# Kernel tuning notes

Measured on AMD Instinct MI355X. Metric: run time of the kernel, lower is better.

## Reference

```python
import jax, jax.numpy as jnp
import numpy as np

B = 1024      # number of samples (sample_idx.shape[0])
H = 256       # hidden_size
E = 64        # number of observation events
NO = 512      # observed samples per event
D = 16        # input_size
ND = 2        # n_dim
S = 4         # euler ODE steps between consecutive events
EPS = 1e-8


def setup_inputs() -> dict:
    key = jax.random.key(0)
    ks = jax.random.split(key, 24)
    X = jax.random.normal(ks[0], (E, NO, D, ND), jnp.float32)
    M = jnp.ones((E, NO, D), jnp.float32)
    rng = np.random.default_rng(0)
    # distinct indices per event (torch scatter temp[i_obs]=... assumes no dup within event)
    batch_idx = jnp.asarray(
        np.stack([rng.permutation(B)[:NO] for _ in range(E)]).astype(np.int32))
    dt = jnp.float32(0.05)
    s = 1.0 / np.sqrt(H)
    def U(k, shp):
        return jax.random.uniform(k, shp, jnp.float32, -s, s)
    inp = {"X": X, "M": M, "batch_idx": batch_idx, "dt": dt}
    # GRU-ODE cell (3 Linear layers H->H, bias init 0.01 in torch; random here)
    inp["ode_Wr"], inp["ode_br"] = U(ks[1], (H, H)), U(ks[2], (H,))
    inp["ode_Wz"], inp["ode_bz"] = U(ks[3], (H, H)), U(ks[4], (H,))
    inp["ode_Wh"], inp["ode_bh"] = U(ks[5], (H, H)), U(ks[6], (H,))
    # GRUCell for observation update: input size 2*D, hidden H
    inp["g_Wxr"], inp["g_Wxz"], inp["g_Wxn"] = U(ks[7], (2 * D, H)), U(ks[8], (2 * D, H)), U(ks[9], (2 * D, H))
    inp["g_Uhr"], inp["g_Uhz"], inp["g_Uhn"] = U(ks[10], (H, H)), U(ks[11], (H, H)), U(ks[12], (H, H))
    inp["g_bxr"], inp["g_bxz"], inp["g_bxn"] = U(ks[13], (H,)), U(ks[14], (H,)), U(ks[15], (H,))
    inp["g_bhr"], inp["g_bhz"], inp["g_bhn"] = U(ks[16], (H,)), U(ks[17], (H,)), U(ks[18], (H,))
    # p_model: Linear(H,H) -> ReLU -> (Dropout p=0, identity in eval) -> Linear(H, D-1)
    inp["p_W1"], inp["p_b1"] = U(ks[19], (H, H)), U(ks[20], (H,))
    inp["p_W2"], inp["p_b2"] = U(ks[21], (H, D - 1)), U(ks[22], (D - 1,))
    return inp


def reference(X, M, batch_idx, dt,
              ode_Wr, ode_br, ode_Wz, ode_bz, ode_Wh, ode_bh,
              g_Wxr, g_Wxz, g_Wxn, g_Uhr, g_Uhz, g_Uhn,
              g_bxr, g_bxz, g_bxn, g_bhr, g_bhz, g_bhn,
              p_W1, p_b1, p_W2, p_b2):
    def euler_step(h):
        r = jax.nn.sigmoid(h @ ode_Wr + ode_br)
        z = jax.nn.sigmoid(h @ ode_Wz + ode_bz)
        u = jnp.tanh((r * h) @ ode_Wh + ode_bh)
        return h + dt * (1.0 - z) * (u - h)

    def event_step(carry, xs):
        h, mse, mae, mape, tot = carry
        Xe, Me, ie = xs                      # [NO,D,ND], [NO,D], [NO]
        for _ in range(S):                   # ODE evolution up to this obs time
            h = euler_step(h)
        p = jax.nn.relu(h @ p_W1 + p_b1) @ p_W2 + p_b2   # [B, D-1]
        Xt = Xe[:, 1:, 0]                    # X_obs[:, :, 0][:, 1:]
        Mt = Me[:, 1:]
        diff = Xt - p[ie]
        mse = mse + jnp.sum(diff * diff * Mt)
        mae = mae + jnp.sum(jnp.abs(diff) * Mt)
        mape = mape + jnp.sum(jnp.abs(diff) / (Xt + EPS) * Mt)
        tot = tot + jnp.sum(Mt)
        # GRUCell observation update, scattered back into h
        x_in = Xe.reshape(Xe.shape[0], -1)   # [NO, 2*D]
        hi = h[ie]                           # [NO, H]
        r = jax.nn.sigmoid(x_in @ g_Wxr + g_bxr + hi @ g_Uhr + g_bhr)
        z = jax.nn.sigmoid(x_in @ g_Wxz + g_bxz + hi @ g_Uhz + g_bhz)
        n = jnp.tanh(x_in @ g_Wxn + g_bxn + r * (hi @ g_Uhn + g_bhn))
        hn = (1.0 - z) * n + z * hi
        h = h.at[ie].set(hn)
        return (h, mse, mae, mape, tot), None

    h0 = jnp.zeros((B, H), jnp.float32)
    zero = jnp.float32(0.0)
    (h, mse, mae, mape, tot), _ = jax.lax.scan(
        event_step, (h0, zero, zero, zero, zero), (X, M, batch_idx))
    return (mse / tot, mae / tot, mape / tot)
```

## Files before the change

kernel.cpp:

```cpp
#include <hip/hip_runtime.h>

#define Bv 1024
#define Ev 64
#define NOv 512
#define L2E  1.44269504088896340736f
#define L2E2 2.88539008177792681472f

typedef _Float16 h8 __attribute__((ext_vector_type(8)));
typedef float f32x4 __attribute__((ext_vector_type(4)));
typedef int i32x8 __attribute__((ext_vector_type(8)));

#define LDH8 272
#define LDA1 264
#define LDX  48

#define MF16(a,b,c) __builtin_amdgcn_mfma_f32_16x16x32_f16((a),(b),(c),0,0,0)
#define MFS(a,b,c) __builtin_amdgcn_mfma_scale_f32_16x16x128_f8f6f4((a),(b),(c),0,0,0,0x7F7F7F7F,0,0x7F7F7F7F)

__device__ __forceinline__ float rcpf(float x) {
    float r; asm("v_rcp_f32 %0, %1" : "=v"(r) : "v"(x)); return r;
}
__device__ __forceinline__ float ex2(float x) {
    float r; asm("v_exp_f32 %0, %1" : "=v"(r) : "v"(x)); return r;
}
__device__ __forceinline__ float sig2(float y) { return rcpf(1.0f + ex2(-y)); }
__device__ __forceinline__ float tanh2(float y) { return fmaf(2.0f, sig2(y), -1.0f); }
__device__ __forceinline__ int pk4_fp8(float a, float b, float c, float d) {
    int p = __builtin_amdgcn_cvt_pk_fp8_f32(a, b, 0, false);
    p = __builtin_amdgcn_cvt_pk_fp8_f32(c, d, p, true);
    return p;
}
__device__ __forceinline__ char fp8b(float v) {
    return (char)(__builtin_amdgcn_cvt_pk_fp8_f32(v, v, 0, false) & 0xff);
}
#define GATHER(dst, A) { \
    float lo_ = sA ? A[1] : A[0]; \
    float hi_ = sA ? A[3] : A[2]; \
    dst = sB ? hi_ : lo_; }

__device__ __forceinline__ i32x8 ld8(const int4* __restrict__ A,
                                     const int4* __restrict__ B, int idx) {
    int4 lo = A[idx], hi = B[idx];
    i32x8 w;
    w[0] = lo.x; w[1] = lo.y; w[2] = lo.z; w[3] = lo.w;
    w[4] = hi.x; w[5] = hi.y; w[6] = hi.z; w[7] = hi.w;
    return w;
}

__device__ __forceinline__ void pack8_body(const float* __restrict__ src,
                                           int4* __restrict__ dst,
                                           int idx, float scale) {
    int lane = idx & 63;
    int kh = (idx >> 6) & 1;
    int ct = idx >> 7;
    int k0 = kh * 128 + (lane >> 4) * 32;
    int n = ct * 16 + (lane & 15);
    int w[8];
    #pragma unroll
    for (int q = 0; q < 8; ++q) {
        float s[4];
        #pragma unroll
        for (int j = 0; j < 4; ++j)
            s[j] = scale * src[(k0 + q * 4 + j) * 256 + n];
        w[q] = pk4_fp8(s[0], s[1], s[2], s[3]);
    }
    dst[idx * 2]     = make_int4(w[0], w[1], w[2], w[3]);
    dst[idx * 2 + 1] = make_int4(w[4], w[5], w[6], w[7]);
}
__device__ __forceinline__ void pack16_body(const float* __restrict__ src,
                                            _Float16* __restrict__ dst,
                                            int idx, int KS, int ncols, float scale) {
    int lane = idx & 63;
    int ks = (idx >> 6) % KS;
    int ct = (idx >> 6) / KS;
    int k0 = ks * 32 + (lane >> 4) * 8;
    int n = ct * 16 + (lane & 15);
    h8 v;
    #pragma unroll
    for (int j = 0; j < 8; ++j)
        v[j] = (n < ncols) ? (_Float16)(scale * src[(k0 + j) * ncols + n]) : (_Float16)0.f;
    ((h8*)dst)[idx] = v;
}

__global__ void prep_all(
    const float* __restrict__ Wr,  const float* __restrict__ Wz,  const float* __restrict__ Wh,
    const float* __restrict__ Uhr, const float* __restrict__ Uhz, const float* __restrict__ Uhn,
    const float* __restrict__ W1,
    const float* __restrict__ Wxr, const float* __restrict__ Wxz, const float* __restrict__ Wxn,
    const float* __restrict__ W2,
    int4* __restrict__ WrQ,  int4* __restrict__ WzQ,  int4* __restrict__ WhQ,
    int4* __restrict__ UhrQ, int4* __restrict__ UhzQ, int4* __restrict__ UhnQ,
    int4* __restrict__ W1Q,
    _Float16* __restrict__ WxrH, _Float16* __restrict__ WxzH, _Float16* __restrict__ WxnH,
    _Float16* __restrict__ W2H,
    int* __restrict__ inv)
{
    int b = blockIdx.x, tid = threadIdx.x;
    if (b < 56) {
        int g = b >> 3;
        int idx = (b & 7) * 256 + tid;
        const float* src; int4* dst; float sc;
        switch (g) {
            case 0: src = Wr;  dst = WrQ;  sc = L2E;  break;
            case 1: src = Wz;  dst = WzQ;  sc = L2E;  break;
            case 2: src = Wh;  dst = WhQ;  sc = L2E2; break;
            case 3: src = Uhr; dst = UhrQ; sc = L2E;  break;
            case 4: src = Uhz; dst = UhzQ; sc = L2E;  break;
            case 5: src = Uhn; dst = UhnQ; sc = L2E2; break;
            default: src = W1; dst = W1Q;  sc = 1.0f; break;
        }
        pack8_body(src, dst, idx, sc);
    } else if (b < 68) {
        int g = (b - 56) >> 2;
        int idx = ((b - 56) & 3) * 256 + tid;
        const float* src; _Float16* dst; float sc;
        switch (g) {
            case 0: src = Wxr; dst = WxrH; sc = L2E;  break;
            case 1: src = Wxz; dst = WxzH; sc = L2E;  break;
            default: src = Wxn; dst = WxnH; sc = L2E2; break;
        }
        pack16_body(src, dst, idx, 1, 256, sc);
    } else if (b < 70) {
        int idx = (b - 68) * 256 + tid;
        if (idx < 512) pack16_body(W2, W2H, idx, 8, 15, 1.0f);
    } else {
        int i = (b - 70) * 256 + tid;
        if (i < Ev * Bv) inv[i] = -1;
    }
}

__global__ void gather_all(const float* __restrict__ X, const float* __restrict__ M,
                           const int* __restrict__ bidx,
                           int* __restrict__ inv, _Float16* __restrict__ Xg,
                           float* __restrict__ Tx, float* __restrict__ Tm)
{
    int b = blockIdx.x, tid = threadIdx.x;
    if (b < 128) {
        int i = b * 256 + tid;
        if (i < Ev * NOv) {
            int e = i >> 9;
            int o = i & (NOv - 1);
            inv[e * Bv + bidx[i]] = o;
        }
    } else if (b < 4224) {
        int i = (b - 128) * 256 + tid;
        if (i < Ev * NOv * 32) {
            int q = i & 31, o = (i >> 5) & (NOv - 1), e = i >> 14;
            int bb = bidx[e * NOv + o];
            Xg[(e * Bv + bb) * 32 + q] = (_Float16)X[i];
        }
    } else {
        int i = (b - 4224) * 256 + tid;
        if (i < Ev * NOv * 16) {
            int m = i & 15, o = (i >> 4) & (NOv - 1), e = i >> 13;
            int bb = bidx[e * NOv + o];
            int d = (e * Bv + bb) * 16 + m;
            if (m < 15) {
                Tx[d] = X[((e * NOv + o) * 16 + 1 + m) * 2];
                Tm[d] = M[(e * NOv + o) * 16 + 1 + m];
            } else {
                Tx[d] = 1.f;
                Tm[d] = 0.f;
            }
        }
    }
}

__global__ __launch_bounds__(1024) void gruode_main(
    const _Float16* __restrict__ Xg, const float* __restrict__ Tx, const float* __restrict__ Tm,
    const float* __restrict__ dtp,
    const float* __restrict__ br, const float* __restrict__ bz, const float* __restrict__ bh,
    const float* __restrict__ bxr, const float* __restrict__ bxz, const float* __restrict__ bxn,
    const float* __restrict__ bhr, const float* __restrict__ bhz, const float* __restrict__ bhn,
    const float* __restrict__ b1, const float* __restrict__ b2,
    const i32x8* __restrict__ WrQ, const i32x8* __restrict__ WzQ, const i32x8* __restrict__ WhQ,
    const i32x8* __restrict__ UhrQ, const i32x8* __restrict__ UhzQ, const i32x8* __restrict__ UhnQ,
    const i32x8* __restrict__ W1Q,
    const h8* __restrict__ WxrH, const h8* __restrict__ WxzH, const h8* __restrict__ WxnH,
    const h8* __restrict__ W2H,
    const int* __restrict__ inv, double* __restrict__ partials)
{
    __shared__ __align__(16) int4     UhrA[2048], UhrB[2048];
    __shared__ __align__(16) int4     UhzA[2048], UhzB[2048];
    __shared__ __align__(16) h8       W2L[512];
    __shared__ __align__(16) char     hb2[2][4 * LDH8];
    __shared__ __align__(16) _Float16 a1s[4 * LDA1];
    __shared__ __align__(16) _Float16 x16d[2][4 * LDX];
    __shared__ __align__(16) float    bias_s[5][256];
    __shared__ __align__(16) float    b2s[16];
    __shared__ int    obsi2[2][16];
    __shared__ double wred[16][4];

    const int tid  = threadIdx.x;
    const int lane = tid & 63;
    const int wid  = tid >> 6;
    const int l16  = lane & 15;
    const int lg   = lane >> 4;
    const int n0   = wid * 16 + lg * 4;
    const int row0 = blockIdx.x * 4;
    const float dtv = dtp[0];
    const int rrow = l16 & 3;

    const int rho = lane & 3;
    const int kap = lane >> 2;
    const int gam = wid * 16 + kap;
    const int hoff = rho * LDH8 + gam;
    const bool sA = (kap & 1) != 0;
    const bool sB = (kap & 2) != 0;
    const int sbase = 64 * lg + 4 * rrow;

    if (tid < 256) {
        bias_s[0][tid] = (bxr[tid] + bhr[tid]) * L2E;
        bias_s[1][tid] = (bxz[tid] + bhz[tid]) * L2E;
        bias_s[2][tid] = bxn[tid] * L2E2;
    } else if (tid < 512) {
        int t = tid - 256;
        bias_s[3][t] = bhn[t] * L2E2;
        bias_s[4][t] = b1[t];
    }
    if (tid < 16) b2s[tid] = (tid < 15) ? b2[tid] : 0.f;
    if (tid < LDH8) {
        ((int*)hb2[0])[tid] = 0;
        ((int*)hb2[1])[tid] = 0;
    }
    for (int i = tid; i < 2048; i += 1024) {
        const int4* s1 = (const int4*)&UhrQ[i];
        UhrA[i] = s1[0]; UhrB[i] = s1[1];
        const int4* s2 = (const int4*)&UhzQ[i];
        UhzA[i] = s2[0]; UhzB[i] = s2[1];
    }
    if (tid < 512) W2L[tid] = W2H[tid];
    if (tid < 16) obsi2[0][tid] = (tid < 4) ? inv[row0 + tid] : -1;
    if (tid < 128) {
        int row = tid >> 5, q = tid & 31;
        x16d[0][row * LDX + q] = Xg[(row0 + row) * 32 + q];
    }

    const float bRs = br[gam] * L2E;
    const float bZs = bz[gam] * L2E;
    const float bUs = bh[gam] * L2E2;

    i32x8 wr0 = WrQ[(wid * 2 + 0) * 64 + lane], wr1 = WrQ[(wid * 2 + 1) * 64 + lane];
    i32x8 wz0 = WzQ[(wid * 2 + 0) * 64 + lane], wz1 = WzQ[(wid * 2 + 1) * 64 + lane];
    i32x8 wh0 = WhQ[(wid * 2 + 0) * 64 + lane], wh1 = WhQ[(wid * 2 + 1) * 64 + lane];

    float hs = 0.f;
    double am0 = 0.0, am1 = 0.0, am2 = 0.0, am3 = 0.0;
    const f32x4 zf = {0.f, 0.f, 0.f, 0.f};
    __syncthreads();

    #pragma unroll 1
    for (int e = 0; e < Ev; ++e) {
        char* __restrict__ HB = hb2[e & 1];
        char* __restrict__ RB = hb2[(e & 1) ^ 1];
        const _Float16* __restrict__ xs = x16d[e & 1];
        const int* __restrict__ obs = obsi2[e & 1];

        float zs = 0.f;
        for (int s = 0; s < 4; ++s) {
            f32x4 aR = zf, aZ = zf;
            {
                i32x8 hb = *(const i32x8*)&HB[rrow * LDH8 + lg * 32];
                aR = MFS(wr0, hb, aR); aZ = MFS(wz0, hb, aZ);
                hb = *(const i32x8*)&HB[rrow * LDH8 + 128 + lg * 32];
                aR = MFS(wr1, hb, aR); aZ = MFS(wz1, hb, aZ);
            }
            float rpre, zpre;
            GATHER(rpre, aR);
            GATHER(zpre, aZ);
            float rv = sig2(rpre + bRs);
            zs = sig2(zpre + bZs);
            RB[hoff] = fp8b(rv * hs);
            __syncthreads();
            f32x4 aU0 = zf, aU1 = zf;
            {
                i32x8 rb = *(const i32x8*)&RB[rrow * LDH8 + lg * 32];
                aU0 = MFS(wh0, rb, aU0);
                rb = *(const i32x8*)&RB[rrow * LDH8 + 128 + lg * 32];
                aU1 = MFS(wh1, rb, aU1);
            }
            float u0, u1;
            GATHER(u0, aU0);
            GATHER(u1, aU1);
            float u = tanh2(u0 + u1 + bUs);
            hs = hs + dtv * (1.f - zs) * (u - hs);
            HB[hoff] = fp8b(hs);
            __syncthreads();
        }
        __builtin_amdgcn_sched_barrier(0);

        i32x8 hb0 = *(const i32x8*)&HB[rrow * LDH8 + lg * 32];
        i32x8 hb1 = *(const i32x8*)&HB[rrow * LDH8 + 128 + lg * 32];
        f32x4 aN = *(const f32x4*)&bias_s[3][n0];
        {
            f32x4 aW = *(const f32x4*)&bias_s[4][n0];
            aN = MFS(UhnQ[(wid * 2 + 0) * 64 + lane], hb0, aN);
            aW = MFS(W1Q[(wid * 2 + 0) * 64 + lane], hb0, aW);
            aN = MFS(UhnQ[(wid * 2 + 1) * 64 + lane], hb1, aN);
            aW = MFS(W1Q[(wid * 2 + 1) * 64 + lane], hb1, aW);
            if (l16 < 4) {
                _Float16 a1v[4];
                #pragma unroll
                for (int r = 0; r < 4; ++r)
                    a1v[r] = (_Float16)fmaxf(aW[r], 0.f);
                *(long*)&a1s[l16 * LDA1 + n0] = *(const long*)a1v;
            }
        }
        {
            int en = (e + 1 < Ev) ? e + 1 : e;
            int nb = (e + 1) & 1;
            if (tid < 16) obsi2[nb][tid] = (tid < 4) ? inv[en * Bv + row0 + tid] : -1;
            if (tid < 128) {
                int row = tid >> 5, q = tid & 31;
                x16d[nb][row * LDX + q] = Xg[(en * Bv + row0 + row) * 32 + q];
            }
        }
        float4 txv = {0.f,0.f,0.f,0.f}, tmv = {0.f,0.f,0.f,0.f};
        if (wid == 0) {
            int gr = row0 + l16; if (gr > Bv - 1) gr = Bv - 1;
            txv = *(const float4*)&Tx[(e * Bv + gr) * 16 + lg * 4];
            tmv = *(const float4*)&Tm[(e * Bv + gr) * 16 + lg * 4];
        }
        float rg[4];
        {
            f32x4 aG = *(const f32x4*)&bias_s[0][n0];
            aG = MFS(ld8(UhrA, UhrB, (wid * 2 + 0) * 64 + lane), hb0, aG);
            aG = MFS(ld8(UhrA, UhrB, (wid * 2 + 1) * 64 + lane), hb1, aG);
            h8 bx = *(const h8*)&xs[rrow * LDX + lg * 8];
            aG = MF16(WxrH[wid * 64 + lane], bx, aG);
            #pragma unroll
            for (int r = 0; r < 4; ++r)
                rg[r] = sig2(aG[r]);
        }
        {
            f32x4 aG = *(const f32x4*)&bias_s[1][n0];
            aG = MFS(ld8(UhzA, UhzB, (wid * 2 + 0) * 64 + lane), hb0, aG);
            aG = MFS(ld8(UhzA, UhzB, (wid * 2 + 1) * 64 + lane), hb1, aG);
            h8 bx = *(const h8*)&xs[rrow * LDX + lg * 8];
            aG = MF16(WxzH[wid * 64 + lane], bx, aG);
            f32x4 aNx = *(const f32x4*)&bias_s[2][n0];
            aNx = MF16(WxnH[wid * 64 + lane], bx, aNx);
            float how[4];
            #pragma unroll
            for (int r = 0; r < 4; ++r)
                how[r] = __int_as_float(__builtin_amdgcn_ds_bpermute(sbase + 16 * r, __float_as_int(hs)));
            float hn[4];
            #pragma unroll
            for (int r = 0; r < 4; ++r) {
                float zg = sig2(aG[r]);
                float nv = tanh2(aNx[r] + rg[r] * aN[r]);
                hn[r] = (1.f - zg) * nv + zg * how[r];
            }
            float hng;
            GATHER(hng, hn);
            if (obs[rho] >= 0) hs = hng;
            RB[hoff] = fp8b(hs);
        }
        __syncthreads();
        if (wid == 0) {
            f32x4 aP = *(const f32x4*)&b2s[lg * 4];
            f32x4 aQ = zf;
            #pragma unroll
            for (int ks = 0; ks < 4; ++ks) {
                h8 ba = *(const h8*)&a1s[rrow * LDA1 + (2 * ks) * 32 + lg * 8];
                aP = MF16(W2L[(2 * ks) * 64 + lane], ba, aP);
                h8 bb = *(const h8*)&a1s[rrow * LDA1 + (2 * ks + 1) * 32 + lg * 8];
                aQ = MF16(W2L[(2 * ks + 1) * 64 + lane], bb, aQ);
            }
            if (obs[l16] >= 0) {
                float m0 = 0.f, m1 = 0.f, m2 = 0.f, m3 = 0.f;
                #pragma unroll
                for (int r = 0; r < 4; ++r) {
                    float p  = aP[r] + aQ[r];
                    float xt = ((const float*)&txv)[r];
                    float mt = ((const float*)&tmv)[r];
                    float diff = xt - p;
                    m0 += diff * diff * mt;
                    m1 += fabsf(diff) * mt;
                    m2 += fabsf(diff) * rcpf(xt + 1e-8f) * mt;
                    m3 += mt;
                }
                am0 += (double)m0;
                am1 += (double)m1;
                am2 += (double)m2;
                am3 += (double)m3;
            }
        }
    }

    __syncthreads();
    double v[4] = {am0, am1, am2, am3};
    #pragma unroll
    for (int m = 0; m < 4; ++m) {
        double t = v[m];
        for (int off = 32; off; off >>= 1) t += __shfl_down(t, off);
        if (lane == 0) wred[wid][m] = t;
    }
    __syncthreads();
    if (tid == 0) {
        for (int m = 0; m < 4; ++m) {
            double t = 0.0;
            for (int w = 0; w < 16; ++w) t += wred[w][m];
            partials[blockIdx.x * 4 + m] = t;
        }
    }
}

__global__ void finalize_k(const double* __restrict__ partials, float* __restrict__ out) {
    __shared__ double sd[4][4];
    int t = threadIdx.x;
    int l = t & 63, w = t >> 6;
    double v0 = partials[t * 4 + 0];
    double v1 = partials[t * 4 + 1];
    double v2 = partials[t * 4 + 2];
    double v3 = partials[t * 4 + 3];
    for (int off = 32; off; off >>= 1) {
        v0 += __shfl_down(v0, off);
        v1 += __shfl_down(v1, off);
        v2 += __shfl_down(v2, off);
        v3 += __shfl_down(v3, off);
    }
    if (l == 0) { sd[w][0] = v0; sd[w][1] = v1; sd[w][2] = v2; sd[w][3] = v3; }
    __syncthreads();
    if (t == 0) {
        double r0 = 0, r1 = 0, r2 = 0, r3 = 0;
        for (int i = 0; i < 4; ++i) { r0 += sd[i][0]; r1 += sd[i][1]; r2 += sd[i][2]; r3 += sd[i][3]; }
        out[0] = (float)(r0 / r3);
        out[1] = (float)(r1 / r3);
        out[2] = (float)(r2 / r3);
    }
}

extern "C" void kernel_launch(void* const* d_in, const int* in_sizes, int n_in,
                              void* d_out, int out_size, void* d_ws, size_t ws_size,
                              hipStream_t stream) {
    const float* X   = (const float*)d_in[0];
    const float* M   = (const float*)d_in[1];
    const int*  bidx = (const int*)d_in[2];
    const float* dtp = (const float*)d_in[3];
    const float* Wr  = (const float*)d_in[4];
    const float* brr = (const float*)d_in[5];
    const float* Wz  = (const float*)d_in[6];
    const float* bzz = (const float*)d_in[7];
    const float* Wh  = (const float*)d_in[8];
    const float* bhh = (const float*)d_in[9];
    const float* Wxr = (const float*)d_in[10];
    const float* Wxz = (const float*)d_in[11];
    const float* Wxn = (const float*)d_in[12];
    const float* Uhr = (const float*)d_in[13];
    const float* Uhz = (const float*)d_in[14];
    const float* Uhn = (const float*)d_in[15];
    const float* bxr = (const float*)d_in[16];
    const float* bxz = (const float*)d_in[17];
    const float* bxn = (const float*)d_in[18];
    const float* bhr = (const float*)d_in[19];
    const float* bhz = (const float*)d_in[20];
    const float* bhn = (const float*)d_in[21];
    const float* W1  = (const float*)d_in[22];
    const float* b1  = (const float*)d_in[23];
    const float* W2  = (const float*)d_in[24];
    const float* b2  = (const float*)d_in[25];

    char* w = (char*)d_ws;
    i32x8* WrQ  = (i32x8*)(w + 0 * 65536);
    i32x8* WzQ  = (i32x8*)(w + 1 * 65536);
    i32x8* WhQ  = (i32x8*)(w + 2 * 65536);
    i32x8* UhrQ = (i32x8*)(w + 3 * 65536);
    i32x8* UhzQ = (i32x8*)(w + 4 * 65536);
    i32x8* UhnQ = (i32x8*)(w + 5 * 65536);
    i32x8* W1Q  = (i32x8*)(w + 6 * 65536);
    _Float16* WxrH = (_Float16*)(w + 458752);
    _Float16* WxzH = (_Float16*)(w + 475136);
    _Float16* WxnH = (_Float16*)(w + 491520);
    _Float16* W2H  = (_Float16*)(w + 507904);
    int* inv = (int*)(w + 516096);
    _Float16* Xg = (_Float16*)(w + 778240);
    float* Tx = (float*)(w + 4972544);
    float* Tm = (float*)(w + 9166848);
    double* partials = (double*)(w + 13361152);

    prep_all<<<326, 256, 0, stream>>>(
        Wr, Wz, Wh, Uhr, Uhz, Uhn, W1, Wxr, Wxz, Wxn, W2,
        (int4*)WrQ, (int4*)WzQ, (int4*)WhQ, (int4*)UhrQ, (int4*)UhzQ,
        (int4*)UhnQ, (int4*)W1Q, WxrH, WxzH, WxnH, W2H, inv);
    gather_all<<<6272, 256, 0, stream>>>(X, M, bidx, inv, Xg, Tx, Tm);

    gruode_main<<<256, 1024, 0, stream>>>(Xg, Tx, Tm, dtp,
        brr, bzz, bhh, bxr, bxz, bxn, bhr, bhz, bhn, b1, b2,
        WrQ, WzQ, WhQ, UhrQ, UhzQ, UhnQ, W1Q,
        (const h8*)WxrH, (const h8*)WxzH, (const h8*)WxnH, (const h8*)W2H,
        inv, partials);

    finalize_k<<<1, 256, 0, stream>>>(partials, (float*)d_out);
}
```

Measured before the change: 441.7 us.

## Halve rows per block, double grid, and stream Uhr/Uhz weights from global

Each block now handles 2 sample rows instead of 4, and the grid doubles to 512 blocks so the 64-event recurrence is spread over more workgroups. The 128 KB LDS staging of the Uhr/Uhz fp8 weights is removed; those MFMA operands are read directly from global memory, with scheduling barriers placed around the gate blocks. The finalize kernel sums 512 partial results instead of 256. The intent is more parallelism per CU at lower LDS use. The costs are that only 2 of the 16 MFMA rows now carry data, the weight reads go through global memory and cache rather than LDS, and if two 1024-thread blocks cannot share a CU, the extra blocks run as a second serial wave.

```diff
diff --git a/kernel.cpp b/kernel.cpp
--- a/kernel.cpp
+++ b/kernel.cpp
@@ -37,15 +37,6 @@
     float lo_ = sA ? A[1] : A[0]; \
     float hi_ = sA ? A[3] : A[2]; \
     dst = sB ? hi_ : lo_; }
-
-__device__ __forceinline__ i32x8 ld8(const int4* __restrict__ A,
-                                     const int4* __restrict__ B, int idx) {
-    int4 lo = A[idx], hi = B[idx];
-    i32x8 w;
-    w[0] = lo.x; w[1] = lo.y; w[2] = lo.z; w[3] = lo.w;
-    w[4] = hi.x; w[5] = hi.y; w[6] = hi.z; w[7] = hi.w;
-    return w;
-}
 
 __device__ __forceinline__ void pack8_body(const float* __restrict__ src,
                                            int4* __restrict__ dst,
@@ -180,12 +171,10 @@
     const h8* __restrict__ W2H,
     const int* __restrict__ inv, double* __restrict__ partials)
 {
-    __shared__ __align__(16) int4     UhrA[2048], UhrB[2048];
-    __shared__ __align__(16) int4     UhzA[2048], UhzB[2048];
     __shared__ __align__(16) h8       W2L[512];
-    __shared__ __align__(16) char     hb2[2][4 * LDH8];
-    __shared__ __align__(16) _Float16 a1s[4 * LDA1];
-    __shared__ __align__(16) _Float16 x16d[2][4 * LDX];
+    __shared__ __align__(16) char     hb2[2][2 * LDH8];
+    __shared__ __align__(16) _Float16 a1s[2 * LDA1];
+    __shared__ __align__(16) _Float16 x16d[2][2 * LDX];
     __shared__ __align__(16) float    bias_s[5][256];
     __shared__ __align__(16) float    b2s[16];
     __shared__ int    obsi2[2][16];
@@ -197,14 +186,14 @@
     const int l16  = lane & 15;
     const int lg   = lane >> 4;
     const int n0   = wid * 16 + lg * 4;
-    const int row0 = blockIdx.x * 4;
+    const int row0 = blockIdx.x * 2;
     const float dtv = dtp[0];
-    const int rrow = l16 & 3;
-
-    const int rho = lane & 3;
+    const int rrow = l16 & 1;
+
+    const int rho2 = lane & 1;
     const int kap = lane >> 2;
     const int gam = wid * 16 + kap;
-    const int hoff = rho * LDH8 + gam;
+    const int hoff = rho2 * LDH8 + gam;
     const bool sA = (kap & 1) != 0;
     const bool sB = (kap & 2) != 0;
     const int sbase = 64 * lg + 4 * rrow;
@@ -219,19 +208,13 @@
         bias_s[4][t] = b1[t];
     }
     if (tid < 16) b2s[tid] = (tid < 15) ? b2[tid] : 0.f;
-    if (tid < LDH8) {
+    if (tid < 136) {
         ((int*)hb2[0])[tid] = 0;
         ((int*)hb2[1])[tid] = 0;
     }
-    for (int i = tid; i < 2048; i += 1024) {
-        const int4* s1 = (const int4*)&UhrQ[i];
-        UhrA[i] = s1[0]; UhrB[i] = s1[1];
-        const int4* s2 = (const int4*)&UhzQ[i];
-        UhzA[i] = s2[0]; UhzB[i] = s2[1];
-    }
     if (tid < 512) W2L[tid] = W2H[tid];
-    if (tid < 16) obsi2[0][tid] = (tid < 4) ? inv[row0 + tid] : -1;
-    if (tid < 128) {
+    if (tid < 16) obsi2[0][tid] = (tid < 2) ? inv[row0 + tid] : -1;
+    if (tid < 64) {
         int row = tid >> 5, q = tid & 31;
         x16d[0][row * LDX + q] = Xg[(row0 + row) * 32 + q];
     }
@@ -298,7 +281,7 @@
             aW = MFS(W1Q[(wid * 2 + 0) * 64 + lane], hb0, aW);
             aN = MFS(UhnQ[(wid * 2 + 1) * 64 + lane], hb1, aN);
             aW = MFS(W1Q[(wid * 2 + 1) * 64 + lane], hb1, aW);
-            if (l16 < 4) {
+            if (l16 < 2) {
                 _Float16 a1v[4];
                 #pragma unroll
                 for (int r = 0; r < 4; ++r)
@@ -309,8 +292,8 @@
         {
             int en = (e + 1 < Ev) ? e + 1 : e;
             int nb = (e + 1) & 1;
-            if (tid < 16) obsi2[nb][tid] = (tid < 4) ? inv[en * Bv + row0 + tid] : -1;
-            if (tid < 128) {
+            if (tid < 16) obsi2[nb][tid] = (tid < 2) ? inv[en * Bv + row0 + tid] : -1;
+            if (tid < 64) {
                 int row = tid >> 5, q = tid & 31;
                 x16d[nb][row * LDX + q] = Xg[(en * Bv + row0 + row) * 32 + q];
             }
@@ -321,21 +304,23 @@
             txv = *(const float4*)&Tx[(e * Bv + gr) * 16 + lg * 4];
             tmv = *(const float4*)&Tm[(e * Bv + gr) * 16 + lg * 4];
         }
+        __builtin_amdgcn_sched_barrier(0);
         float rg[4];
         {
             f32x4 aG = *(const f32x4*)&bias_s[0][n0];
-            aG = MFS(ld8(UhrA, UhrB, (wid * 2 + 0) * 64 + lane), hb0, aG);
-            aG = MFS(ld8(UhrA, UhrB, (wid * 2 + 1) * 64 + lane), hb1, aG);
+            aG = MFS(UhrQ[(wid * 2 + 0) * 64 + lane], hb0, aG);
+            aG = MFS(UhrQ[(wid * 2 + 1) * 64 + lane], hb1, aG);
             h8 bx = *(const h8*)&xs[rrow * LDX + lg * 8];
             aG = MF16(WxrH[wid * 64 + lane], bx, aG);
             #pragma unroll
             for (int r = 0; r < 4; ++r)
                 rg[r] = sig2(aG[r]);
         }
+        __builtin_amdgcn_sched_barrier(0);
         {
             f32x4 aG = *(const f32x4*)&bias_s[1][n0];
-            aG = MFS(ld8(UhzA, UhzB, (wid * 2 + 0) * 64 + lane), hb0, aG);
-            aG = MFS(ld8(UhzA, UhzB, (wid * 2 + 1) * 64 + lane), hb1, aG);
+            aG = MFS(UhzQ[(wid * 2 + 0) * 64 + lane], hb0, aG);
+            aG = MFS(UhzQ[(wid * 2 + 1) * 64 + lane], hb1, aG);
             h8 bx = *(const h8*)&xs[rrow * LDX + lg * 8];
             aG = MF16(WxzH[wid * 64 + lane], bx, aG);
             f32x4 aNx = *(const f32x4*)&bias_s[2][n0];
@@ -353,7 +338,7 @@
             }
             float hng;
             GATHER(hng, hn);
-            if (obs[rho] >= 0) hs = hng;
+            if (obs[rho2] >= 0) hs = hng;
             RB[hoff] = fp8b(hs);
         }
         __syncthreads();
@@ -410,10 +395,10 @@
     __shared__ double sd[4][4];
     int t = threadIdx.x;
     int l = t & 63, w = t >> 6;
-    double v0 = partials[t * 4 + 0];
-    double v1 = partials[t * 4 + 1];
-    double v2 = partials[t * 4 + 2];
-    double v3 = partials[t * 4 + 3];
+    double v0 = partials[t * 4 + 0] + partials[(t + 256) * 4 + 0];
+    double v1 = partials[t * 4 + 1] + partials[(t + 256) * 4 + 1];
+    double v2 = partials[t * 4 + 2] + partials[(t + 256) * 4 + 2];
+    double v3 = partials[t * 4 + 3] + partials[(t + 256) * 4 + 3];
     for (int off = 32; off; off >>= 1) {
         v0 += __shfl_down(v0, off);
         v1 += __shfl_down(v1, off);
@@ -485,7 +470,7 @@
         (int4*)UhnQ, (int4*)W1Q, WxrH, WxzH, WxnH, W2H, inv);
     gather_all<<<6272, 256, 0, stream>>>(X, M, bidx, inv, Xg, Tx, Tm);
 
-    gruode_main<<<256, 1024, 0, stream>>>(Xg, Tx, Tm, dtp,
+    gruode_main<<<512, 1024, 0, stream>>>(Xg, Tx, Tm, dtp,
         brr, bzz, bhh, bxr, bxz, bxn, bhr, bhz, bhn, b1, b2,
         WrQ, WzQ, WhQ, UhrQ, UhzQ, UhnQ, W1Q,
         (const h8*)WxrH, (const h8*)WxzH, (const h8*)WxnH, (const h8*)W2H,
```

New measurement: 1.075 ms. +143.4%, slower.
